# Performance work log

Measured on AMD Instinct MI355X. Metric: run time of the kernel, lower is better.

The kernel has to match this reference:

```python
import jax, jax.numpy as jnp
import numpy as np

INPUT_DIM = 2048
CLASSES = 1000
BATCH = 8192


def setup_inputs() -> dict:
    key = jax.random.key(0)
    kx, ky, kwx, kbx, kwy, kby = jax.random.split(key, 6)
    s_in = 1.0 / np.sqrt(INPUT_DIM)
    return {
        "x": jax.random.normal(kx, (BATCH, INPUT_DIM), dtype=jnp.float32),
        "y": jax.random.normal(ky, (BATCH, INPUT_DIM), dtype=jnp.float32),
        "Wx": jax.random.uniform(kwx, (CLASSES, INPUT_DIM), jnp.float32, -s_in, s_in),
        "bx": jax.random.uniform(kbx, (CLASSES,), jnp.float32, -s_in, s_in),
        "Wy": jax.random.uniform(kwy, (CLASSES, INPUT_DIM), jnp.float32, -s_in, s_in),
        "by": jax.random.uniform(kby, (CLASSES,), jnp.float32, -s_in, s_in),
    }


def _ds_combin_two(alpha1, alpha2, classes):
    # alpha1, alpha2: [B, C] Dirichlet params
    S1 = jnp.sum(alpha1, axis=1, keepdims=True)  # [B,1]
    S2 = jnp.sum(alpha2, axis=1, keepdims=True)
    b1 = (alpha1 - 1.0) / S1                      # belief masses [B,C]
    b2 = (alpha2 - 1.0) / S2
    u1 = classes / S1                             # uncertainty [B,1]
    u2 = classes / S2
    # bb_sum = sum_{i,j} b1_i b2_j = (sum b1)(sum b2); bb_diag = sum_i b1_i b2_i
    bb_sum = jnp.sum(b1, axis=1) * jnp.sum(b2, axis=1)   # [B]
    bb_diag = jnp.sum(b1 * b2, axis=1)                    # [B]
    C = (bb_sum - bb_diag)[:, None]                       # conflict [B,1]
    denom = 1.0 - C
    b_a = (b1 * b2 + b1 * u2 + b2 * u1) / denom           # [B,C]
    u_a = (u1 * u2) / denom                               # [B,1]
    S_a = classes / u_a                                   # [B,1]
    return b_a * S_a + 1.0                                # alpha_a [B,C]


def reference(x, y, Wx, bx, Wy, by):
    out_x = x @ Wx.T + bx                 # [B,C]
    out_y = y @ Wy.T + by
    alpha_x = jax.nn.softplus(out_x) + 1.0
    alpha_y = jax.nn.softplus(out_y) + 1.0
    alpha_a = _ds_combin_two(alpha_x, alpha_y, CLASSES)
    return (alpha_a, alpha_x, alpha_y)
```

## Files before the change

### kernel.cpp

```cpp
#include <hip/hip_runtime.h>
#include <hip/hip_bf16.h>
#include <math.h>

#define BATCH_N 8192
#define K_DIM   2048
#define CLS     1000
#define NPAD    1024

typedef __attribute__((ext_vector_type(8))) short short8;
typedef __attribute__((ext_vector_type(8))) unsigned short ushort8;
typedef __attribute__((ext_vector_type(4))) float floatx4;

static __device__ __forceinline__ ushort f2bf(float f) {
    union { float f; unsigned u; } v; v.f = f;
    unsigned u = v.u;
    return (ushort)((u + 0x7FFFu + ((u >> 16) & 1u)) >> 16);
}

static __device__ __forceinline__ void gld_lds16(const void* g, void* l) {
    __builtin_amdgcn_global_load_lds(
        (const __attribute__((address_space(1))) void*)g,
        (__attribute__((address_space(3))) void*)l, 16, 0, 0);
}

static __device__ __forceinline__ float softplus_fast(float z) {
    return fmaxf(z, 0.f) + __logf(1.f + __expf(-fabsf(z)));
}

__global__ __launch_bounds__(256)
void convert_all(const float* __restrict__ x, const float* __restrict__ y,
                 const float* __restrict__ wx, const float* __restrict__ wy,
                 ushort* __restrict__ xb, ushort* __restrict__ yb,
                 ushort* __restrict__ wxb, ushort* __restrict__ wyb)
{
    int b = blockIdx.x;
    const float* src; ushort* dst; bool isw = false;
    if (b < 8192)       { src = x;  dst = xb; }
    else if (b < 16384) { src = y;  dst = yb;  b -= 8192; }
    else if (b < 17408) { src = wx; dst = wxb; b -= 16384; isw = true; }
    else                { src = wy; dst = wyb; b -= 17408; isw = true; }
    size_t e = ((size_t)b * 256 + threadIdx.x) * 8;
    ushort8 t = (ushort8)0;
    if (!isw || (int)(e >> 11) < CLS) {
        float4 a = *(const float4*)(src + e);
        float4 c = *(const float4*)(src + e + 4);
#pragma unroll
        for (int j = 0; j < 4; ++j) {
            t[j]     = f2bf(((const float*)&a)[j]);
            t[j + 4] = f2bf(((const float*)&c)[j]);
        }
    }
    *(ushort8*)(dst + e) = t;
}


constexpr int NT = K_DIM / 64;

#define BARX __builtin_amdgcn_s_barrier()
#define LGKM0 asm volatile("s_waitcnt lgkmcnt(0)" ::: "memory")
#define VMW(n) asm volatile("s_waitcnt vmcnt(" #n ")" ::: "memory")
#define PRIO1 __builtin_amdgcn_s_setprio(1)
#define PRIO0 __builtin_amdgcn_s_setprio(0)

#define STAGE_A(h, sl, t_) {                                                  \
    const size_t kb_ = (size_t)(t_) * 64;                                     \
    gld_lds16(A + aofs_g[0] + (h) * 64 * K_DIM + kb_,                         \
              &As[sl][aofs_l[0] + (h) * 4096]);                               \
    gld_lds16(A + aofs_g[1] + (h) * 64 * K_DIM + kb_,                         \
              &As[sl][aofs_l[1] + (h) * 4096]); }
#define STAGE_B(h, sl, t_) {                                                  \
    const size_t kb_ = (size_t)(t_) * 64;                                     \
    gld_lds16(B + bofs_g[0] + (h) * 32 * K_DIM + kb_,                         \
              &Bs[sl][bofs_l[0] + (h) * 2048]);                               \
    gld_lds16(B + bofs_g[1] + (h) * 32 * K_DIM + kb_,                         \
              &Bs[sl][bofs_l[1] + (h) * 2048]); }

#define LDA(mh) {                                                             \
    const ushort* p_ = asl + wr * 8192 + (mh) * 4096;                         \
    a[0][0] = *(const short8*)(p_ + e0);        a[0][1] = *(const short8*)(p_ + e1); \
    a[1][0] = *(const short8*)(p_ + 1024 + e0); a[1][1] = *(const short8*)(p_ + 1024 + e1); \
    a[2][0] = *(const short8*)(p_ + 2048 + e0); a[2][1] = *(const short8*)(p_ + 2048 + e1); \
    a[3][0] = *(const short8*)(p_ + 3072 + e0); a[3][1] = *(const short8*)(p_ + 3072 + e1); }
#define LDB(nh, bb) {                                                         \
    const ushort* p_ = bsl + wc * 4096 + (nh) * 2048;                         \
    bb[0][0] = *(const short8*)(p_ + e0);        bb[0][1] = *(const short8*)(p_ + e1); \
    bb[1][0] = *(const short8*)(p_ + 1024 + e0); bb[1][1] = *(const short8*)(p_ + 1024 + e1); }

#define MM1(mh, nh, i, j, kk, bb)                                             \
    acc[(mh)*4+(i)][(nh)*2+(j)] = __builtin_amdgcn_mfma_f32_16x16x32_bf16(    \
        a[i][kk], bb[j][kk], acc[(mh)*4+(i)][(nh)*2+(j)], 0, 0, 0);
#define MQ(mh, nh, bb)                                                        \
    MM1(mh,nh,0,0,0,bb) MM1(mh,nh,0,1,0,bb) MM1(mh,nh,1,0,0,bb) MM1(mh,nh,1,1,0,bb) \
    MM1(mh,nh,2,0,0,bb) MM1(mh,nh,2,1,0,bb) MM1(mh,nh,3,0,0,bb) MM1(mh,nh,3,1,0,bb) \
    MM1(mh,nh,0,0,1,bb) MM1(mh,nh,0,1,1,bb) MM1(mh,nh,1,0,1,bb) MM1(mh,nh,1,1,1,bb) \
    MM1(mh,nh,2,0,1,bb) MM1(mh,nh,2,1,1,bb) MM1(mh,nh,3,0,1,bb) MM1(mh,nh,3,1,1,bb)

__global__ __launch_bounds__(512, 2)
void gemm8p(const ushort* __restrict__ Aa, const ushort* __restrict__ Ab,
            const ushort* __restrict__ Ba, const ushort* __restrict__ Bb,
            const float* __restrict__ biasa, const float* __restrict__ biasb,
            float* __restrict__ outa, float* __restrict__ outb)
{
    int flat = blockIdx.x + 4 * (blockIdx.y + 32 * blockIdx.z);
    int sw   = (flat & 7) * 32 + (flat >> 3);
    const int bx = sw & 3, by = (sw >> 2) & 31, bz = sw >> 7;

    const ushort* A   = bz ? Ab : Aa;
    const ushort* B   = bz ? Bb : Ba;
    const float* bias = bz ? biasb : biasa;
    float* out        = bz ? outb : outa;

    __shared__ ushort As[2][256 * 64];
    __shared__ ushort Bs[2][256 * 64];

    const int tid  = threadIdx.x;
    const int lane = tid & 63;
    const int wid  = tid >> 6;
    const int wr = wid >> 2, wc = wid & 3;
    const int fr = lane & 15, fg = lane >> 4;
    const int frx8 = (fr & 7) << 3;
    const int brow = by * 256;
    const int bcol = bx * 256;

    int    aofs_l[2], bofs_l[2];
    size_t aofs_g[2], bofs_g[2];
#pragma unroll
    for (int i = 0; i < 2; ++i) {
        int q = i * 512 + tid, rr = q >> 3, c8 = q & 7, c8l = c8 ^ (rr & 7);
        int ra = (rr >> 6) * 128 + (rr & 63);
        int rb = (rr >> 5) * 64  + (rr & 31);
        aofs_l[i] = ra * 64 + c8 * 8;
        bofs_l[i] = rb * 64 + c8 * 8;
        aofs_g[i] = (size_t)(brow + ra) * K_DIM + c8l * 8;
        bofs_g[i] = (size_t)(bcol + rb) * K_DIM + c8l * 8;
    }

    const int e0 = fr * 64 + ((fg * 8) ^ frx8);
    const int e1 = fr * 64 + ((32 + fg * 8) ^ frx8);

    floatx4 acc[8][4];
#pragma unroll
    for (int m = 0; m < 8; ++m)
#pragma unroll
        for (int n = 0; n < 4; ++n)
            acc[m][n] = (floatx4){0.f, 0.f, 0.f, 0.f};

    STAGE_A(0, 0, 0) STAGE_B(0, 0, 0) STAGE_B(1, 0, 0) STAGE_A(1, 0, 0)
    STAGE_A(0, 1, 1) STAGE_B(0, 1, 1)
    VMW(6); BARX;

    short8 a[4][2], bl[2][2], bh[2][2];

#pragma unroll 1
    for (int t = 0; t < NT - 2; ++t) {
        const int sl = t & 1, sl1 = sl ^ 1;
        const ushort* asl = &As[sl][0];
        const ushort* bsl = &Bs[sl][0];
        LDA(0) LDB(0, bl)
        STAGE_B(1, sl1, t + 1)
        BARX; LGKM0;
        PRIO1; MQ(0, 0, bl) PRIO0;
        VMW(6); BARX;
        LDB(1, bh)
        STAGE_A(1, sl1, t + 1)
        BARX; LGKM0;
        PRIO1; MQ(0, 1, bh) PRIO0;
        BARX;
        LDA(1)
        STAGE_A(0, sl, t + 2)
        BARX; LGKM0;
        PRIO1; MQ(1, 1, bh) PRIO0;
        BARX;
        STAGE_B(0, sl, t + 2)
        BARX; LGKM0;
        PRIO1; MQ(1, 0, bl) PRIO0;
        VMW(6); BARX;
    }
    {
        const int sl = (NT - 2) & 1, sl1 = sl ^ 1;
        const ushort* asl = &As[sl][0];
        const ushort* bsl = &Bs[sl][0];
        LDA(0) LDB(0, bl)
        STAGE_B(1, sl1, NT - 1)
        BARX; LGKM0; PRIO1; MQ(0, 0, bl) PRIO0; VMW(6); BARX;
        LDB(1, bh)
        STAGE_A(1, sl1, NT - 1)
        BARX; LGKM0; PRIO1; MQ(0, 1, bh) PRIO0; BARX;
        LDA(1)
        BARX; LGKM0; PRIO1; MQ(1, 1, bh) PRIO0; BARX;
        BARX; LGKM0; PRIO1; MQ(1, 0, bl) PRIO0; VMW(2); BARX;
    }
    {
        const int sl = (NT - 1) & 1;
        const ushort* asl = &As[sl][0];
        const ushort* bsl = &Bs[sl][0];
        LDA(0) LDB(0, bl)
        BARX; LGKM0; PRIO1; MQ(0, 0, bl) PRIO0; VMW(0); BARX;
        LDB(1, bh)
        BARX; LGKM0; PRIO1; MQ(0, 1, bh) PRIO0; BARX;
        LDA(1)
        BARX; LGKM0; PRIO1; MQ(1, 1, bh) PRIO0; BARX;
        LGKM0; PRIO1; MQ(1, 0, bl) PRIO0;
    }

#pragma unroll
    for (int n = 0; n < 4; ++n) {
        int col = bcol + wc * 64 + n * 16 + fr;
        if (col >= CLS) continue;
        float bv = bias[col];
#pragma unroll
        for (int m = 0; m < 8; ++m) {
#pragma unroll
            for (int j = 0; j < 4; ++j) {
                int row = brow + wr * 128 + m * 16 + fg * 4 + j;
                float z = acc[m][n][j] + bv;
                out[(size_t)row * CLS + col] = softplus_fast(z) + 1.f;
            }
        }
    }
}


constexpr int FBM = 128, FBN = 128, FBK = 64;
constexpr int FNKT = K_DIM / FBK;
constexpr int LDP = FBK + 8;

__global__ __launch_bounds__(256, 2)
void gemm_alpha(const float* __restrict__ Xa, const float* __restrict__ Xb,
                const float* __restrict__ Wa, const float* __restrict__ Wb,
                const float* __restrict__ ba, const float* __restrict__ bb,
                float* __restrict__ outa, float* __restrict__ outb)
{
    const float* X   = blockIdx.z ? Xb : Xa;
    const float* W   = blockIdx.z ? Wb : Wa;
    const float* bias= blockIdx.z ? bb : ba;
    float* out       = blockIdx.z ? outb : outa;

    __shared__ ushort As[FBM][LDP];
    __shared__ ushort Bs[FBN][LDP];

    const int tid  = threadIdx.x;
    const int brow = blockIdx.y * FBM;
    const int bcol = blockIdx.x * FBN;

    float4 ra[4][2], rb[4][2];

    auto load_tile = [&](int kt) {
        const int kbase = kt * FBK;
#pragma unroll
        for (int i = 0; i < 4; ++i) {
            int idx = tid + i * 256;
            int row = idx >> 3;
            int c8  = (idx & 7) << 3;
            const float* pA = X + (size_t)(brow + row) * K_DIM + kbase + c8;
            ra[i][0] = *(const float4*)pA;
            ra[i][1] = *(const float4*)(pA + 4);
            int wrow = bcol + row; if (wrow >= CLS) wrow = CLS - 1;
            const float* pB = W + (size_t)wrow * K_DIM + kbase + c8;
            rb[i][0] = *(const float4*)pB;
            rb[i][1] = *(const float4*)(pB + 4);
        }
    };

    auto store_tile = [&]() {
#pragma unroll
        for (int i = 0; i < 4; ++i) {
            int idx = tid + i * 256;
            int row = idx >> 3;
            int c8  = (idx & 7) << 3;
            ushort8 ta, tb;
#pragma unroll
            for (int j = 0; j < 4; ++j) {
                ta[j]     = f2bf(((const float*)&ra[i][0])[j]);
                ta[j + 4] = f2bf(((const float*)&ra[i][1])[j]);
                tb[j]     = f2bf(((const float*)&rb[i][0])[j]);
                tb[j + 4] = f2bf(((const float*)&rb[i][1])[j]);
            }
            *(ushort8*)&As[row][c8] = ta;
            *(ushort8*)&Bs[row][c8] = tb;
        }
    };

    const int lane = tid & 63;
    const int wid  = tid >> 6;
    const int wr = wid >> 1, wc = wid & 1;
    const int row0 = wr * 64, col0 = wc * 64;
    const int fr = lane & 15;
    const int fg = lane >> 4;

    floatx4 acc[4][4];
#pragma unroll
    for (int m = 0; m < 4; ++m)
#pragma unroll
        for (int n = 0; n < 4; ++n)
            acc[m][n] = (floatx4){0.f, 0.f, 0.f, 0.f};

    load_tile(0);
    for (int kt = 0; kt < FNKT; ++kt) {
        if (kt) __syncthreads();
        store_tile();
        __syncthreads();
        if (kt + 1 < FNKT) load_tile(kt + 1);
#pragma unroll
        for (int kk = 0; kk < 2; ++kk) {
            short8 af[4], bf8[4];
#pragma unroll
            for (int m = 0; m < 4; ++m)
                af[m] = *(const short8*)&As[row0 + m * 16 + fr][kk * 32 + fg * 8];
#pragma unroll
            for (int n = 0; n < 4; ++n)
                bf8[n] = *(const short8*)&Bs[col0 + n * 16 + fr][kk * 32 + fg * 8];
#pragma unroll
            for (int m = 0; m < 4; ++m)
#pragma unroll
                for (int n = 0; n < 4; ++n)
                    acc[m][n] = __builtin_amdgcn_mfma_f32_16x16x32_bf16(
                        af[m], bf8[n], acc[m][n], 0, 0, 0);
        }
    }

#pragma unroll
    for (int n = 0; n < 4; ++n) {
        int col = bcol + col0 + n * 16 + fr;
        if (col >= CLS) continue;
        float bv = bias[col];
#pragma unroll
        for (int m = 0; m < 4; ++m) {
#pragma unroll
            for (int j = 0; j < 4; ++j) {
                int row = brow + row0 + m * 16 + fg * 4 + j;
                float z = acc[m][n][j] + bv;
                out[(size_t)row * CLS + col] = softplus_fast(z) + 1.f;
            }
        }
    }
}


__global__ __launch_bounds__(256)
void ds_combine(const float* __restrict__ AX, const float* __restrict__ AY,
                float* __restrict__ out)
{
    const int row = blockIdx.x * 4 + (threadIdx.x >> 6);
    const int l = threadIdx.x & 63;
    const float* ax = AX + (size_t)row * CLS;
    const float* ay = AY + (size_t)row * CLS;

    float4 vx[4], vy[4];
    float sx = 0.f, sy = 0.f, sp = 0.f;
#pragma unroll
    for (int c = 0; c < 4; ++c) {
        int idx = l + c * 64;
        if (idx < CLS / 4) {
            vx[c] = *(const float4*)(ax + idx * 4);
            vy[c] = *(const float4*)(ay + idx * 4);
            const float* px = (const float*)&vx[c];
            const float* py = (const float*)&vy[c];
#pragma unroll
            for (int j = 0; j < 4; ++j) {
                sx += px[j]; sy += py[j];
                sp += (px[j] - 1.f) * (py[j] - 1.f);
            }
        }
    }
#pragma unroll
    for (int off = 1; off < 64; off <<= 1) {
        sx += __shfl_xor(sx, off);
        sy += __shfl_xor(sy, off);
        sp += __shfl_xor(sp, off);
    }
    const float S1 = sx, S2 = sy, P = sp;
    const float i1 = 1.f / S1, i2 = 1.f / S2;
    const float u1 = (float)CLS * i1, u2 = (float)CLS * i2;
    const float sb1 = (S1 - (float)CLS) * i1;
    const float sb2 = (S2 - (float)CLS) * i2;
    const float conf = sb1 * sb2 - P * i1 * i2;
    const float denom = 1.f - conf;
    const float idenom = 1.f / denom;
    const float Sa = (float)CLS * denom / (u1 * u2);

#pragma unroll
    for (int c = 0; c < 4; ++c) {
        int idx = l + c * 64;
        if (idx < CLS / 4) {
            float4 vo;
            const float* px = (const float*)&vx[c];
            const float* py = (const float*)&vy[c];
            float* po = (float*)&vo;
#pragma unroll
            for (int j = 0; j < 4; ++j) {
                float b1 = (px[j] - 1.f) * i1;
                float b2 = (py[j] - 1.f) * i2;
                float ba = (b1 * b2 + b1 * u2 + b2 * u1) * idenom;
                po[j] = ba * Sa + 1.f;
            }
            *(float4*)(out + (size_t)row * CLS + idx * 4) = vo;
        }
    }
}

extern "C" void kernel_launch(void* const* d_in, const int* in_sizes, int n_in,
                              void* d_out, int out_size, void* d_ws, size_t ws_size,
                              hipStream_t stream) {
    const float* x  = (const float*)d_in[0];
    const float* y  = (const float*)d_in[1];
    const float* Wx = (const float*)d_in[2];
    const float* bx = (const float*)d_in[3];
    const float* Wy = (const float*)d_in[4];
    const float* by = (const float*)d_in[5];
    float* out = (float*)d_out;
    float* ax = out + (size_t)BATCH_N * CLS;
    float* ay = ax  + (size_t)BATCH_N * CLS;

    const size_t SZ_X = (size_t)BATCH_N * K_DIM;
    const size_t SZ_W = (size_t)NPAD * K_DIM;
    const size_t need = (2 * SZ_X + 2 * SZ_W) * sizeof(ushort);

    if (ws_size >= need) {
        ushort* xb  = (ushort*)d_ws;
        ushort* yb  = xb + SZ_X;
        ushort* wxb = yb + SZ_X;
        ushort* wyb = wxb + SZ_W;

        convert_all<<<18432, 256, 0, stream>>>(x, y, Wx, Wy, xb, yb, wxb, wyb);
        gemm8p<<<dim3(NPAD / 256, BATCH_N / 256, 2), 512, 0, stream>>>(
            xb, yb, wxb, wyb, bx, by, ax, ay);
    } else {
        gemm_alpha<<<dim3((CLS + FBN - 1) / FBN, BATCH_N / FBM, 2), 256, 0, stream>>>(
            x, y, Wx, Wy, bx, by, ax, ay);
    }
    ds_combine<<<BATCH_N / 4, 256, 0, stream>>>(ax, ay, out);
}
```

Measured before the change: 133.4 us.

## Software-pipeline LDS fragment loads across MFMA phases with double-buffered registers

Restructures the gemm8p main loop so LDS-to-register fragment loads for the next quarter-tile (and the next k-tile) are issued before the current MFMA block. Partial lgkmcnt waits replace full waits, and A/B fragments get double-buffered register sets. The loop is unrolled by two to alternate buffers statically. This aims to hide LDS read latency behind MFMA execution, at the cost of more VGPRs, which may hurt occupancy under launch_bounds(512,2). Shared arrays in the fallback kernel are renamed without functional change.

Result: slower. 172.0 us (+28.9%).

```diff
diff --git a/kernel.cpp b/kernel.cpp
--- a/kernel.cpp
+++ b/kernel.cpp
@@ -57,8 +57,8 @@
 constexpr int NT = K_DIM / 64;
 
 #define BARX __builtin_amdgcn_s_barrier()
-#define LGKM0 asm volatile("s_waitcnt lgkmcnt(0)" ::: "memory")
-#define VMW(n) asm volatile("s_waitcnt vmcnt(" #n ")" ::: "memory")
+#define LGKMW(n) asm volatile("s_waitcnt lgkmcnt(" #n ")" ::: "memory")
+#define VMW(n)   asm volatile("s_waitcnt vmcnt(" #n ")" ::: "memory")
 #define PRIO1 __builtin_amdgcn_s_setprio(1)
 #define PRIO0 __builtin_amdgcn_s_setprio(0)
 
@@ -75,25 +75,51 @@
     gld_lds16(B + bofs_g[1] + (h) * 32 * K_DIM + kb_,                         \
               &Bs[sl][bofs_l[1] + (h) * 2048]); }
 
-#define LDA(mh) {                                                             \
-    const ushort* p_ = asl + wr * 8192 + (mh) * 4096;                         \
-    a[0][0] = *(const short8*)(p_ + e0);        a[0][1] = *(const short8*)(p_ + e1); \
-    a[1][0] = *(const short8*)(p_ + 1024 + e0); a[1][1] = *(const short8*)(p_ + 1024 + e1); \
-    a[2][0] = *(const short8*)(p_ + 2048 + e0); a[2][1] = *(const short8*)(p_ + 2048 + e1); \
-    a[3][0] = *(const short8*)(p_ + 3072 + e0); a[3][1] = *(const short8*)(p_ + 3072 + e1); }
-#define LDB(nh, bb) {                                                         \
-    const ushort* p_ = bsl + wc * 4096 + (nh) * 2048;                         \
-    bb[0][0] = *(const short8*)(p_ + e0);        bb[0][1] = *(const short8*)(p_ + e1); \
-    bb[1][0] = *(const short8*)(p_ + 1024 + e0); bb[1][1] = *(const short8*)(p_ + 1024 + e1); }
-
-#define MM1(mh, nh, i, j, kk, bb)                                             \
+#define LDA_LO(dst, base, h) {                                                \
+    const ushort* p_ = (base) + wr * 8192 + (h) * 4096;                       \
+    dst[0][0] = *(const short8*)(p_ + e0);        dst[0][1] = *(const short8*)(p_ + e1); \
+    dst[1][0] = *(const short8*)(p_ + 1024 + e0); dst[1][1] = *(const short8*)(p_ + 1024 + e1); }
+#define LDA_HI(dst, base, h) {                                                \
+    const ushort* p_ = (base) + wr * 8192 + (h) * 4096;                       \
+    dst[2][0] = *(const short8*)(p_ + 2048 + e0); dst[2][1] = *(const short8*)(p_ + 2048 + e1); \
+    dst[3][0] = *(const short8*)(p_ + 3072 + e0); dst[3][1] = *(const short8*)(p_ + 3072 + e1); }
+#define LDA_ALL(dst, base, h) LDA_LO(dst, base, h) LDA_HI(dst, base, h)
+#define LDB_TO(dst, base, h) {                                                \
+    const ushort* p_ = (base) + wc * 4096 + (h) * 2048;                       \
+    dst[0][0] = *(const short8*)(p_ + e0);        dst[0][1] = *(const short8*)(p_ + e1); \
+    dst[1][0] = *(const short8*)(p_ + 1024 + e0); dst[1][1] = *(const short8*)(p_ + 1024 + e1); }
+
+#define MM(mh, nh, i, j, kk, Ar, Br)                                          \
     acc[(mh)*4+(i)][(nh)*2+(j)] = __builtin_amdgcn_mfma_f32_16x16x32_bf16(    \
-        a[i][kk], bb[j][kk], acc[(mh)*4+(i)][(nh)*2+(j)], 0, 0, 0);
-#define MQ(mh, nh, bb)                                                        \
-    MM1(mh,nh,0,0,0,bb) MM1(mh,nh,0,1,0,bb) MM1(mh,nh,1,0,0,bb) MM1(mh,nh,1,1,0,bb) \
-    MM1(mh,nh,2,0,0,bb) MM1(mh,nh,2,1,0,bb) MM1(mh,nh,3,0,0,bb) MM1(mh,nh,3,1,0,bb) \
-    MM1(mh,nh,0,0,1,bb) MM1(mh,nh,0,1,1,bb) MM1(mh,nh,1,0,1,bb) MM1(mh,nh,1,1,1,bb) \
-    MM1(mh,nh,2,0,1,bb) MM1(mh,nh,2,1,1,bb) MM1(mh,nh,3,0,1,bb) MM1(mh,nh,3,1,1,bb)
+        Ar[i][kk], Br[j][kk], acc[(mh)*4+(i)][(nh)*2+(j)], 0, 0, 0);
+#define MQ(mh, nh, Ar, Br)                                                    \
+    MM(mh,nh,0,0,0,Ar,Br) MM(mh,nh,0,1,0,Ar,Br) MM(mh,nh,1,0,0,Ar,Br) MM(mh,nh,1,1,0,Ar,Br) \
+    MM(mh,nh,2,0,0,Ar,Br) MM(mh,nh,2,1,0,Ar,Br) MM(mh,nh,3,0,0,Ar,Br) MM(mh,nh,3,1,0,Ar,Br) \
+    MM(mh,nh,0,0,1,Ar,Br) MM(mh,nh,0,1,1,Ar,Br) MM(mh,nh,1,0,1,Ar,Br) MM(mh,nh,1,1,1,Ar,Br) \
+    MM(mh,nh,2,0,1,Ar,Br) MM(mh,nh,2,1,1,Ar,Br) MM(mh,nh,3,0,1,Ar,Br) MM(mh,nh,3,1,1,Ar,Br)
+
+#define TILE_STEADY(t_, sl_, sl1_, BLc, BLn)                                  \
+    STAGE_B(1, sl1_, (t_) + 1)                                                \
+    LDB_TO(bh, &Bs[sl_][0], 1)                                                \
+    BARX; LGKMW(4);                                                           \
+    PRIO1; MQ(0, 0, a0, BLc) PRIO0;                                           \
+    VMW(6); BARX;                                                             \
+    STAGE_A(1, sl1_, (t_) + 1)                                                \
+    LDA_ALL(a1, &As[sl_][0], 1)                                               \
+    BARX; LGKMW(8);                                                           \
+    PRIO1; MQ(0, 1, a0, bh) PRIO0;                                            \
+    VMW(4); BARX;                                                             \
+    STAGE_A(0, sl_, (t_) + 2)                                                 \
+    LDB_TO(BLn, &Bs[sl1_][0], 0)                                              \
+    LDA_LO(a0, &As[sl1_][0], 0)                                               \
+    BARX; LGKMW(8);                                                           \
+    PRIO1; MQ(1, 1, a1, bh) PRIO0;                                            \
+    BARX;                                                                     \
+    STAGE_B(0, sl_, (t_) + 2)                                                 \
+    LDA_HI(a0, &As[sl1_][0], 0)                                               \
+    BARX;                                                                     \
+    PRIO1; MQ(1, 0, a1, BLc) PRIO0;                                           \
+    VMW(6); BARX;
 
 __global__ __launch_bounds__(512, 2)
 void gemm8p(const ushort* __restrict__ Aa, const ushort* __restrict__ Ab,
@@ -145,62 +171,53 @@
         for (int n = 0; n < 4; ++n)
             acc[m][n] = (floatx4){0.f, 0.f, 0.f, 0.f};
 
+    short8 a0[4][2], a1[4][2], bh[2][2], blA[2][2], blB[2][2];
+
     STAGE_A(0, 0, 0) STAGE_B(0, 0, 0) STAGE_B(1, 0, 0) STAGE_A(1, 0, 0)
     STAGE_A(0, 1, 1) STAGE_B(0, 1, 1)
     VMW(6); BARX;
-
-    short8 a[4][2], bl[2][2], bh[2][2];
+    LDB_TO(blA, &Bs[0][0], 0)
+    LDA_ALL(a0, &As[0][0], 0)
 
 #pragma unroll 1
-    for (int t = 0; t < NT - 2; ++t) {
-        const int sl = t & 1, sl1 = sl ^ 1;
-        const ushort* asl = &As[sl][0];
-        const ushort* bsl = &Bs[sl][0];
-        LDA(0) LDB(0, bl)
-        STAGE_B(1, sl1, t + 1)
-        BARX; LGKM0;
-        PRIO1; MQ(0, 0, bl) PRIO0;
+    for (int tt = 0; tt < (NT - 2) / 2; ++tt) {
+        TILE_STEADY(2 * tt,     0, 1, blA, blB)
+        TILE_STEADY(2 * tt + 1, 1, 0, blB, blA)
+    }
+    {
+        STAGE_B(1, 1, 31)
+        LDB_TO(bh, &Bs[0][0], 1)
+        BARX; LGKMW(4);
+        PRIO1; MQ(0, 0, a0, blA) PRIO0;
         VMW(6); BARX;
-        LDB(1, bh)
-        STAGE_A(1, sl1, t + 1)
-        BARX; LGKM0;
-        PRIO1; MQ(0, 1, bh) PRIO0;
+        STAGE_A(1, 1, 31)
+        LDA_ALL(a1, &As[0][0], 1)
+        BARX; LGKMW(8);
+        PRIO1; MQ(0, 1, a0, bh) PRIO0;
+        VMW(4); BARX;
+        LDB_TO(blB, &Bs[1][0], 0)
+        LDA_LO(a0, &As[1][0], 0)
+        BARX; LGKMW(8);
+        PRIO1; MQ(1, 1, a1, bh) PRIO0;
         BARX;
-        LDA(1)
-        STAGE_A(0, sl, t + 2)
-        BARX; LGKM0;
-        PRIO1; MQ(1, 1, bh) PRIO0;
+        LDA_HI(a0, &As[1][0], 0)
         BARX;
-        STAGE_B(0, sl, t + 2)
-        BARX; LGKM0;
-        PRIO1; MQ(1, 0, bl) PRIO0;
-        VMW(6); BARX;
+        PRIO1; MQ(1, 0, a1, blA) PRIO0;
+        VMW(2); BARX;
     }
     {
-        const int sl = (NT - 2) & 1, sl1 = sl ^ 1;
-        const ushort* asl = &As[sl][0];
-        const ushort* bsl = &Bs[sl][0];
-        LDA(0) LDB(0, bl)
-        STAGE_B(1, sl1, NT - 1)
-        BARX; LGKM0; PRIO1; MQ(0, 0, bl) PRIO0; VMW(6); BARX;
-        LDB(1, bh)
-        STAGE_A(1, sl1, NT - 1)
-        BARX; LGKM0; PRIO1; MQ(0, 1, bh) PRIO0; BARX;
-        LDA(1)
-        BARX; LGKM0; PRIO1; MQ(1, 1, bh) PRIO0; BARX;
-        BARX; LGKM0; PRIO1; MQ(1, 0, bl) PRIO0; VMW(2); BARX;
-    }
-    {
-        const int sl = (NT - 1) & 1;
-        const ushort* asl = &As[sl][0];
-        const ushort* bsl = &Bs[sl][0];
-        LDA(0) LDB(0, bl)
-        BARX; LGKM0; PRIO1; MQ(0, 0, bl) PRIO0; VMW(0); BARX;
-        LDB(1, bh)
-        BARX; LGKM0; PRIO1; MQ(0, 1, bh) PRIO0; BARX;
-        LDA(1)
-        BARX; LGKM0; PRIO1; MQ(1, 1, bh) PRIO0; BARX;
-        LGKM0; PRIO1; MQ(1, 0, bl) PRIO0;
+        LDB_TO(bh, &Bs[1][0], 1)
+        BARX; LGKMW(4);
+        PRIO1; MQ(0, 0, a0, blB) PRIO0;
+        VMW(0); BARX;
+        LDA_ALL(a1, &As[1][0], 1)
+        BARX; LGKMW(8);
+        PRIO1; MQ(0, 1, a0, bh) PRIO0;
+        BARX;
+        BARX; LGKMW(0);
+        PRIO1; MQ(1, 1, a1, bh) PRIO0;
+        BARX;
+        PRIO1; MQ(1, 0, a1, blB) PRIO0;
     }
 
 #pragma unroll
@@ -236,8 +253,8 @@
     const float* bias= blockIdx.z ? bb : ba;
     float* out       = blockIdx.z ? outb : outa;
 
-    __shared__ ushort As[FBM][LDP];
-    __shared__ ushort Bs[FBN][LDP];
+    __shared__ ushort Asf[FBM][LDP];
+    __shared__ ushort Bsf[FBN][LDP];
 
     const int tid  = threadIdx.x;
     const int brow = blockIdx.y * FBM;
@@ -276,8 +293,8 @@
                 tb[j]     = f2bf(((const float*)&rb[i][0])[j]);
                 tb[j + 4] = f2bf(((const float*)&rb[i][1])[j]);
             }
-            *(ushort8*)&As[row][c8] = ta;
-            *(ushort8*)&Bs[row][c8] = tb;
+            *(ushort8*)&Asf[row][c8] = ta;
+            *(ushort8*)&Bsf[row][c8] = tb;
         }
     };
 
@@ -306,10 +323,10 @@
             short8 af[4], bf8[4];
 #pragma unroll
             for (int m = 0; m < 4; ++m)
-                af[m] = *(const short8*)&As[row0 + m * 16 + fr][kk * 32 + fg * 8];
+                af[m] = *(const short8*)&Asf[row0 + m * 16 + fr][kk * 32 + fg * 8];
 #pragma unroll
             for (int n = 0; n < 4; ++n)
-                bf8[n] = *(const short8*)&Bs[col0 + n * 16 + fr][kk * 32 + fg * 8];
+                bf8[n] = *(const short8*)&Bsf[col0 + n * 16 + fr][kk * 32 + fg * 8];
 #pragma unroll
             for (int m = 0; m < 4; ++m)
 #pragma unroll
```
